# Kernel tuning notes

Measured on AMD Instinct MI355X. Metric: run time of the kernel, lower is better.

## Reference

```python
import jax, jax.numpy as jnp
import numpy as np

B = 32768
INPUT_DIM = 2048
D = 2
HIDDEN = 128
V = 20          # output_dim (number of heads)
P = 6           # n_corr_params
R = 10          # r_lora = min(V // 2, 10)


def setup_inputs() -> dict:
    key = jax.random.key(0)
    ks = jax.random.split(key, 12)

    def lin(k, fan_in, shape):
        bound = 1.0 / np.sqrt(fan_in)
        return jax.random.uniform(k, shape, jnp.float32, -bound, bound)

    x = jax.random.normal(ks[0], (B, INPUT_DIM), jnp.float32)
    # encoder: Linear(input_dim, hidden) -> ReLU -> (Dropout=id) -> Linear(hidden, d)
    We1 = lin(ks[1], INPUT_DIM, (INPUT_DIM, HIDDEN))
    be1 = lin(ks[2], INPUT_DIM, (HIDDEN,))
    We2 = lin(ks[3], HIDDEN, (HIDDEN, D))
    be2 = lin(ks[4], HIDDEN, (D,))
    # 20 heads, each Linear(d, hidden) -> ReLU -> Linear(hidden, 6) -> Tanh,
    # stacked into batched weight tensors.
    W1 = lin(ks[5], D, (V, D, HIDDEN))
    b1 = lin(ks[6], D, (V, HIDDEN))
    W2 = lin(ks[7], HIDDEN, (V, HIDDEN, P))
    b2 = lin(ks[8], HIDDEN, (V, P))
    # LoRA params
    lora_A = jax.random.normal(ks[9], (D, R), jnp.float32) * 0.01
    lora_B = jax.random.normal(ks[10], (R, V * P), jnp.float32) * 0.01
    return {"x": x, "We1": We1, "be1": be1, "We2": We2, "be2": be2,
            "W1": W1, "b1": b1, "W2": W2, "b2": b2,
            "lora_A": lora_A, "lora_B": lora_B}


def reference(x, We1, be1, We2, be2, W1, b1, W2, b2, lora_A, lora_B):
    # encoder (nonlinear reduction; dropout is identity in eval)
    z = jax.nn.relu(x @ We1 + be1) @ We2 + be2            # [B, D]
    # all 20 heads as batched GEMMs
    h = jax.nn.relu(jnp.einsum('bd,vdh->bvh', z, W1) + b1)  # [B, V, HIDDEN]
    heads = jnp.tanh(jnp.einsum('bvh,vhp->bvp', h, W2) + b2)  # [B, V, P]
    # LoRA contribution, then outer tanh (note: double tanh, faithful to source)
    lora = (z @ lora_A @ lora_B).reshape(-1, V, P)         # [B, V, P]
    out = jnp.tanh(heads + 0.15 * lora)
    return (out, z)
```

## Files before the change

### kernel.cpp

```cpp
#include <hip/hip_runtime.h>
#include <hip/hip_bf16.h>
#include <cstdint>
#include <cstddef>

#define BDIM   32768
#define KDIM   2048
#define NDIM   128
#define VHEADS 20
#define PDIM   6
#define RLORA  10

#define BK      64
#define NCHUNK  (KDIM / BK)
#define OUT_ELEMS   (BDIM * VHEADS * PDIM)
#define WS_W_BYTES  (KDIM * NDIM * 2)

typedef __attribute__((ext_vector_type(8))) __bf16 bf16x8;
typedef __attribute__((ext_vector_type(4))) float f32x4;
typedef __attribute__((ext_vector_type(2))) float f32x2;
typedef __attribute__((ext_vector_type(4))) unsigned int u32x4;

union FragU { bf16x8 b; u32x4 u; };

__device__ __forceinline__ unsigned int cvt_pk_bf16(float lo, float hi) {
  unsigned int r;
  asm("v_cvt_pk_bf16_f32 %0, %1, %2" : "=v"(r) : "v"(lo), "v"(hi));
  return r;
}

__device__ __forceinline__ void gload_lds16(const void* g, void* l) {
  __builtin_amdgcn_global_load_lds(
      (const __attribute__((address_space(1))) void*)(g),
      (__attribute__((address_space(3))) void*)(l), 16, 0, 0);
}

__device__ __forceinline__ float fast_tanh(float x) {
  float ax = fabsf(x);
  float e  = __expf(-2.0f * ax);
  float t  = __fdividef(1.0f - e, 1.0f + e);
  return copysignf(t, x);
}

__global__ __launch_bounds__(256)
void k0_pack(const float* __restrict__ We1,
             const float* __restrict__ lA,
             const float* __restrict__ lB,
             unsigned short* __restrict__ wsw,
             float* __restrict__ wsM) {
  if (blockIdx.x == 128) {
    int t = threadIdx.x;
    if (t < 2 * VHEADS * PDIM) {
      int d  = t / (VHEADS * PDIM);
      int vp = t - d * (VHEADS * PDIM);
      float s = 0.f;
#pragma unroll
      for (int r = 0; r < RLORA; ++r)
        s = fmaf(lA[d * RLORA + r], lB[r * (VHEADS * PDIM) + vp], s);
      wsM[t] = s;
    }
    return;
  }
  int t    = blockIdx.x * 256 + threadIdx.x;
  int lane = t & 63;
  int blk  = t >> 6;
  int ks   = blk & 1;
  int nt   = (blk >> 1) & 7;
  int c    = blk >> 4;
  int n    = nt * 16 + (lane & 15);
  int kb   = c * BK + ks * 32 + (lane >> 4) * 8;

  unsigned int u[4];
#pragma unroll
  for (int q = 0; q < 4; ++q) {
    float f0 = We1[(size_t)(kb + 2 * q + 0) * NDIM + n];
    float f1 = We1[(size_t)(kb + 2 * q + 1) * NDIM + n];
    __hip_bfloat16 h0 = __float2bfloat16(f0);
    __hip_bfloat16 h1 = __float2bfloat16(f1);
    u[q] = (unsigned int)*reinterpret_cast<unsigned short*>(&h0) |
           ((unsigned int)*reinterpret_cast<unsigned short*>(&h1) << 16);
  }
  *reinterpret_cast<u32x4*>(wsw + (size_t)t * 8) = u32x4{u[0], u[1], u[2], u[3]};
}

__global__ __launch_bounds__(256, 2)
void k1_fused(const float* __restrict__ x,
              const unsigned short* __restrict__ wp,
              const float* __restrict__ be1,
              const float* __restrict__ We2,
              const float* __restrict__ be2,
              const float* __restrict__ W1,
              const float* __restrict__ b1,
              const float* __restrict__ W2,
              const float* __restrict__ b2,
              const float* __restrict__ M,
              float* __restrict__ out,
              float* __restrict__ zout) {
  __shared__ char ldsA[2][16384] __attribute__((aligned(16)));
  __shared__ char ldsB[2][16384] __attribute__((aligned(16)));
  __shared__ float zsh[64][2];

  const int tid  = threadIdx.x;
  const int lane = tid & 63;
  const int wv   = tid >> 6;
  const int l15  = lane & 15;
  const int kgrp = lane >> 4;
  const int blk  = blockIdx.x;

  const int arow_off = wv * 16 + (lane >> 4);
  const char* bsrc = (const char*)wp + lane * 16;

  f32x4 acc[8];
#pragma unroll
  for (int i = 0; i < 8; ++i) acc[i] = f32x4{0.f, 0.f, 0.f, 0.f};

  auto STAGE = [&](int b, int c) {
#pragma unroll
    for (int q = 0; q < 4; ++q) {
      int row = arow_off + q * 4;
      const float* asrc = x + ((size_t)(blk * 64 + row) * KDIM + c * BK
                               + (((l15 ^ (row & 7)) << 2)));
      gload_lds16(asrc, &ldsA[b][(wv * 4 + q) * 1024]);
    }
#pragma unroll
    for (int q = 0; q < 4; ++q) {
      gload_lds16(bsrc + (size_t)c * 16384 + (wv * 4 + q) * 1024,
                  &ldsB[b][(wv * 4 + q) * 1024]);
    }
  };

  auto COMPUTE = [&](int b) {
    const int row = wv * 16 + l15;
    const char* abase = &ldsA[b][row * 256];
    const int rx = (row & 7) << 4;
    f32x4 A0 = *(const f32x4*)(abase + (((kgrp * 2 + 0) << 4) ^ rx));
    f32x4 A1 = *(const f32x4*)(abase + (((kgrp * 2 + 1) << 4) ^ rx));
    f32x4 A2 = *(const f32x4*)(abase + 128 + (((kgrp * 2 + 0) << 4) ^ rx));
    f32x4 A3 = *(const f32x4*)(abase + 128 + (((kgrp * 2 + 1) << 4) ^ rx));
    FragU a0, a1;
    a0.u = u32x4{cvt_pk_bf16(A0.x, A0.y), cvt_pk_bf16(A0.z, A0.w),
                 cvt_pk_bf16(A1.x, A1.y), cvt_pk_bf16(A1.z, A1.w)};
    a1.u = u32x4{cvt_pk_bf16(A2.x, A2.y), cvt_pk_bf16(A2.z, A2.w),
                 cvt_pk_bf16(A3.x, A3.y), cvt_pk_bf16(A3.z, A3.w)};
    const char* bbase = &ldsB[b][lane * 16];
#pragma unroll
    for (int nt = 0; nt < 8; ++nt) {
      FragU b0, b1;
      b0.u = *(const u32x4*)(bbase + (nt * 2 + 0) * 1024);
      b1.u = *(const u32x4*)(bbase + (nt * 2 + 1) * 1024);
      acc[nt] = __builtin_amdgcn_mfma_f32_16x16x32_bf16(a0.b, b0.b, acc[nt], 0, 0, 0);
      acc[nt] = __builtin_amdgcn_mfma_f32_16x16x32_bf16(a1.b, b1.b, acc[nt], 0, 0, 0);
    }
  };

  STAGE(0, 0);
  __syncthreads();

#pragma unroll 2
  for (int c = 0; c < NCHUNK; ++c) {
    int b = c & 1;
    if (c + 1 < NCHUNK) STAGE(b ^ 1, c + 1);
    COMPUTE(b);
    __syncthreads();
  }

  float part[4][2];
#pragma unroll
  for (int j = 0; j < 4; ++j) { part[j][0] = 0.f; part[j][1] = 0.f; }
#pragma unroll
  for (int nt = 0; nt < 8; ++nt) {
    int col = nt * 16 + l15;
    float bb = be1[col];
    float w0 = We2[col * 2 + 0];
    float w1 = We2[col * 2 + 1];
#pragma unroll
    for (int j = 0; j < 4; ++j) {
      float h = acc[nt][j] + bb;
      h = h > 0.f ? h : 0.f;
      part[j][0] = fmaf(h, w0, part[j][0]);
      part[j][1] = fmaf(h, w1, part[j][1]);
    }
  }
#pragma unroll
  for (int m = 1; m < 16; m <<= 1) {
#pragma unroll
    for (int j = 0; j < 4; ++j) {
      part[j][0] += __shfl_xor(part[j][0], m, 64);
      part[j][1] += __shfl_xor(part[j][1], m, 64);
    }
  }
  if (l15 == 0) {
    float bz0 = be2[0], bz1 = be2[1];
#pragma unroll
    for (int j = 0; j < 4; ++j) {
      int rl = wv * 16 + kgrp * 4 + j;
      float zz0 = part[j][0] + bz0;
      float zz1 = part[j][1] + bz1;
      zsh[rl][0] = zz0;
      zsh[rl][1] = zz1;
      f32x2 zz = {zz0, zz1};
      *(f32x2*)(zout + (size_t)(blk * 64 + rl) * 2) = zz;
    }
  }
  __syncthreads();

  const int wvu = __builtin_amdgcn_readfirstlane(wv);
  float z0 = zsh[lane][0];
  float z1 = zsh[lane][1];
  float* orow = out + (size_t)(blk * 64 + lane) * (VHEADS * PDIM);

#pragma unroll 1
  for (int i = 0; i < 5; ++i) {
    int v = i * 4 + wvu;
    const float* w1a = W1 + (size_t)(v * 2 + 0) * NDIM;
    const float* w1b = W1 + (size_t)(v * 2 + 1) * NDIM;
    const float* bb1 = b1 + (size_t)v * NDIM;
    const float* w2  = W2 + (size_t)v * NDIM * PDIM;

    float p[6] = {0.f, 0.f, 0.f, 0.f, 0.f, 0.f};
#pragma unroll 4
    for (int h = 0; h < NDIM; ++h) {
      float hv = fmaf(z0, w1a[h], fmaf(z1, w1b[h], bb1[h]));
      hv = hv > 0.f ? hv : 0.f;
#pragma unroll
      for (int j = 0; j < 6; ++j) p[j] = fmaf(hv, w2[h * 6 + j], p[j]);
    }
    float o[6];
#pragma unroll
    for (int j = 0; j < 6; ++j) {
      float t1 = fast_tanh(p[j] + b2[v * PDIM + j]);
      float lo = fmaf(z0, M[v * PDIM + j], z1 * M[VHEADS * PDIM + v * PDIM + j]);
      o[j] = fast_tanh(fmaf(0.15f, lo, t1));
    }
    float* op = orow + v * PDIM;
    f32x2 o01 = {o[0], o[1]};
    f32x2 o23 = {o[2], o[3]};
    f32x2 o45 = {o[4], o[5]};
    __builtin_nontemporal_store(o01, (f32x2*)(op + 0));
    __builtin_nontemporal_store(o23, (f32x2*)(op + 2));
    __builtin_nontemporal_store(o45, (f32x2*)(op + 4));
  }
}

extern "C" void kernel_launch(void* const* d_in, const int* in_sizes, int n_in,
                              void* d_out, int out_size, void* d_ws, size_t ws_size,
                              hipStream_t stream) {
  const float* x   = (const float*)d_in[0];
  const float* We1 = (const float*)d_in[1];
  const float* be1 = (const float*)d_in[2];
  const float* We2 = (const float*)d_in[3];
  const float* be2 = (const float*)d_in[4];
  const float* W1  = (const float*)d_in[5];
  const float* b1  = (const float*)d_in[6];
  const float* W2  = (const float*)d_in[7];
  const float* b2  = (const float*)d_in[8];
  const float* lA  = (const float*)d_in[9];
  const float* lB  = (const float*)d_in[10];

  float* out  = (float*)d_out;
  float* zout = out + OUT_ELEMS;
  unsigned short* wsw = (unsigned short*)d_ws;
  float* wsM = (float*)((char*)d_ws + WS_W_BYTES);

  hipLaunchKernelGGL(k0_pack, dim3(129), dim3(256), 0, stream,
                     We1, lA, lB, wsw, wsM);
  hipLaunchKernelGGL(k1_fused, dim3(BDIM / 64), dim3(256), 0, stream,
                     x, wsw, be1, We2, be2, W1, b1, W2, b2, wsM, out, zout);
}
```

Measured before the change: 116.9 us.

## Shrink row tile to 16 and split hidden columns across waves with direct B loads

Reduces the per-block row tile from 64 to 16 rows, giving 2048 blocks, and splits the 128 hidden columns across the four waves, each wave holding two 16-column accumulators. The packed bf16 weights are now read straight from global memory into registers instead of being staged through LDS. The K chunk grows to 128. Per-wave partial z values are reduced through shared memory, and the head stage spreads the 20 heads over 16 slots of 16 rows. The aim is more occupancy and parallelism with less LDS traffic, at the cost of re-reading the weight matrix from L2 four times as often and adding an extra cross-wave reduction barrier.

```diff
diff --git a/kernel.cpp b/kernel.cpp
--- a/kernel.cpp
+++ b/kernel.cpp
@@ -10,8 +10,9 @@
 #define PDIM   6
 #define RLORA  10
 
-#define BK      64
-#define NCHUNK  (KDIM / BK)
+#define BM     16
+#define BK2    128
+#define NCH    (KDIM / BK2)
 #define OUT_ELEMS   (BDIM * VHEADS * PDIM)
 #define WS_W_BYTES  (KDIM * NDIM * 2)
 
@@ -67,7 +68,7 @@
   int nt   = (blk >> 1) & 7;
   int c    = blk >> 4;
   int n    = nt * 16 + (lane & 15);
-  int kb   = c * BK + ks * 32 + (lane >> 4) * 8;
+  int kb   = c * 64 + ks * 32 + (lane >> 4) * 8;
 
   unsigned int u[4];
 #pragma unroll
@@ -82,7 +83,7 @@
   *reinterpret_cast<u32x4*>(wsw + (size_t)t * 8) = u32x4{u[0], u[1], u[2], u[3]};
 }
 
-__global__ __launch_bounds__(256, 2)
+__global__ __launch_bounds__(256, 4)
 void k1_fused(const float* __restrict__ x,
               const unsigned short* __restrict__ wp,
               const float* __restrict__ be1,
@@ -95,9 +96,9 @@
               const float* __restrict__ M,
               float* __restrict__ out,
               float* __restrict__ zout) {
-  __shared__ char ldsA[2][16384] __attribute__((aligned(16)));
-  __shared__ char ldsB[2][16384] __attribute__((aligned(16)));
-  __shared__ float zsh[64][2];
+  __shared__ float ldsA[2][2048] __attribute__((aligned(16)));
+  __shared__ float zpart[4][16][2];
+  __shared__ float zsh[16][2];
 
   const int tid  = threadIdx.x;
   const int lane = tid & 63;
@@ -106,60 +107,56 @@
   const int kgrp = lane >> 4;
   const int blk  = blockIdx.x;
 
-  const int arow_off = wv * 16 + (lane >> 4);
-  const char* bsrc = (const char*)wp + lane * 16;
-
-  f32x4 acc[8];
-#pragma unroll
-  for (int i = 0; i < 8; ++i) acc[i] = f32x4{0.f, 0.f, 0.f, 0.f};
+  const float* arow = x + (size_t)(blk * BM + wv * 4 + (lane >> 4)) * KDIM
+                        + (lane & 15) * 4;
+
+  f32x4 acc[2];
+  acc[0] = f32x4{0.f, 0.f, 0.f, 0.f};
+  acc[1] = f32x4{0.f, 0.f, 0.f, 0.f};
 
   auto STAGE = [&](int b, int c) {
-#pragma unroll
-    for (int q = 0; q < 4; ++q) {
-      int row = arow_off + q * 4;
-      const float* asrc = x + ((size_t)(blk * 64 + row) * KDIM + c * BK
-                               + (((l15 ^ (row & 7)) << 2)));
-      gload_lds16(asrc, &ldsA[b][(wv * 4 + q) * 1024]);
-    }
-#pragma unroll
-    for (int q = 0; q < 4; ++q) {
-      gload_lds16(bsrc + (size_t)c * 16384 + (wv * 4 + q) * 1024,
-                  &ldsB[b][(wv * 4 + q) * 1024]);
-    }
+    const float* s0 = arow + c * BK2;
+    gload_lds16(s0,      &ldsA[b][wv * 256]);
+    gload_lds16(s0 + 64, &ldsA[b][1024 + wv * 256]);
   };
 
-  auto COMPUTE = [&](int b) {
-    const int row = wv * 16 + l15;
-    const char* abase = &ldsA[b][row * 256];
-    const int rx = (row & 7) << 4;
-    f32x4 A0 = *(const f32x4*)(abase + (((kgrp * 2 + 0) << 4) ^ rx));
-    f32x4 A1 = *(const f32x4*)(abase + (((kgrp * 2 + 1) << 4) ^ rx));
-    f32x4 A2 = *(const f32x4*)(abase + 128 + (((kgrp * 2 + 0) << 4) ^ rx));
-    f32x4 A3 = *(const f32x4*)(abase + 128 + (((kgrp * 2 + 1) << 4) ^ rx));
-    FragU a0, a1;
-    a0.u = u32x4{cvt_pk_bf16(A0.x, A0.y), cvt_pk_bf16(A0.z, A0.w),
-                 cvt_pk_bf16(A1.x, A1.y), cvt_pk_bf16(A1.z, A1.w)};
-    a1.u = u32x4{cvt_pk_bf16(A2.x, A2.y), cvt_pk_bf16(A2.z, A2.w),
-                 cvt_pk_bf16(A3.x, A3.y), cvt_pk_bf16(A3.z, A3.w)};
-    const char* bbase = &ldsB[b][lane * 16];
-#pragma unroll
-    for (int nt = 0; nt < 8; ++nt) {
-      FragU b0, b1;
-      b0.u = *(const u32x4*)(bbase + (nt * 2 + 0) * 1024);
-      b1.u = *(const u32x4*)(bbase + (nt * 2 + 1) * 1024);
-      acc[nt] = __builtin_amdgcn_mfma_f32_16x16x32_bf16(a0.b, b0.b, acc[nt], 0, 0, 0);
-      acc[nt] = __builtin_amdgcn_mfma_f32_16x16x32_bf16(a1.b, b1.b, acc[nt], 0, 0, 0);
+  auto COMPUTE = [&](int b, int c) {
+    const char* bb = (const char*)wp + (size_t)c * 32768 + lane * 16;
+    FragU bf[2][4];
+#pragma unroll
+    for (int ntl = 0; ntl < 2; ++ntl) {
+      int nt = wv * 2 + ntl;
+#pragma unroll
+      for (int ks = 0; ks < 4; ++ks) {
+        int off = (((ks >> 1) * 16) + nt * 2 + (ks & 1)) * 1024;
+        bf[ntl][ks].u = *(const u32x4*)(bb + off);
+      }
+    }
+    const char* ab = (const char*)&ldsA[b][0] + l15 * 256 + kgrp * 32;
+    FragU af[4];
+#pragma unroll
+    for (int ks = 0; ks < 4; ++ks) {
+      const char* p = ab + (ks & 1) * 128 + (ks >> 1) * 4096;
+      f32x4 lo = *(const f32x4*)(p);
+      f32x4 hi = *(const f32x4*)(p + 16);
+      af[ks].u = u32x4{cvt_pk_bf16(lo.x, lo.y), cvt_pk_bf16(lo.z, lo.w),
+                       cvt_pk_bf16(hi.x, hi.y), cvt_pk_bf16(hi.z, hi.w)};
+    }
+#pragma unroll
+    for (int ks = 0; ks < 4; ++ks) {
+      acc[0] = __builtin_amdgcn_mfma_f32_16x16x32_bf16(af[ks].b, bf[0][ks].b, acc[0], 0, 0, 0);
+      acc[1] = __builtin_amdgcn_mfma_f32_16x16x32_bf16(af[ks].b, bf[1][ks].b, acc[1], 0, 0, 0);
     }
   };
 
   STAGE(0, 0);
   __syncthreads();
 
-#pragma unroll 2
-  for (int c = 0; c < NCHUNK; ++c) {
+#pragma unroll 1
+  for (int c = 0; c < NCH; ++c) {
     int b = c & 1;
-    if (c + 1 < NCHUNK) STAGE(b ^ 1, c + 1);
-    COMPUTE(b);
+    if (c + 1 < NCH) STAGE(b ^ 1, c + 1);
+    COMPUTE(b, c);
     __syncthreads();
   }
 
@@ -167,14 +164,14 @@
 #pragma unroll
   for (int j = 0; j < 4; ++j) { part[j][0] = 0.f; part[j][1] = 0.f; }
 #pragma unroll
-  for (int nt = 0; nt < 8; ++nt) {
-    int col = nt * 16 + l15;
+  for (int ntl = 0; ntl < 2; ++ntl) {
+    int col = (wv * 2 + ntl) * 16 + l15;
     float bb = be1[col];
     float w0 = We2[col * 2 + 0];
     float w1 = We2[col * 2 + 1];
 #pragma unroll
     for (int j = 0; j < 4; ++j) {
-      float h = acc[nt][j] + bb;
+      float h = acc[ntl][j] + bb;
       h = h > 0.f ? h : 0.f;
       part[j][0] = fmaf(h, w0, part[j][0]);
       part[j][1] = fmaf(h, w1, part[j][1]);
@@ -189,28 +186,32 @@
     }
   }
   if (l15 == 0) {
-    float bz0 = be2[0], bz1 = be2[1];
 #pragma unroll
     for (int j = 0; j < 4; ++j) {
-      int rl = wv * 16 + kgrp * 4 + j;
-      float zz0 = part[j][0] + bz0;
-      float zz1 = part[j][1] + bz1;
-      zsh[rl][0] = zz0;
-      zsh[rl][1] = zz1;
-      f32x2 zz = {zz0, zz1};
-      *(f32x2*)(zout + (size_t)(blk * 64 + rl) * 2) = zz;
+      zpart[wv][kgrp * 4 + j][0] = part[j][0];
+      zpart[wv][kgrp * 4 + j][1] = part[j][1];
     }
   }
   __syncthreads();
-
-  const int wvu = __builtin_amdgcn_readfirstlane(wv);
-  float z0 = zsh[lane][0];
-  float z1 = zsh[lane][1];
-  float* orow = out + (size_t)(blk * 64 + lane) * (VHEADS * PDIM);
-
-#pragma unroll 1
-  for (int i = 0; i < 5; ++i) {
-    int v = i * 4 + wvu;
+  if (tid < BM) {
+    float s0 = zpart[0][tid][0] + zpart[1][tid][0] + zpart[2][tid][0] +
+               zpart[3][tid][0] + be2[0];
+    float s1 = zpart[0][tid][1] + zpart[1][tid][1] + zpart[2][tid][1] +
+               zpart[3][tid][1] + be2[1];
+    zsh[tid][0] = s0;
+    zsh[tid][1] = s1;
+    f32x2 zz = {s0, s1};
+    *(f32x2*)(zout + (size_t)(blk * BM + tid) * 2) = zz;
+  }
+  __syncthreads();
+
+  const int srow = tid & 15;
+  const int slot = tid >> 4;
+  float z0 = zsh[srow][0];
+  float z1 = zsh[srow][1];
+  float* orow = out + (size_t)(blk * BM + srow) * (VHEADS * PDIM);
+
+  auto head = [&](int v) {
     const float* w1a = W1 + (size_t)(v * 2 + 0) * NDIM;
     const float* w1b = W1 + (size_t)(v * 2 + 1) * NDIM;
     const float* bb1 = b1 + (size_t)v * NDIM;
@@ -238,7 +239,10 @@
     __builtin_nontemporal_store(o01, (f32x2*)(op + 0));
     __builtin_nontemporal_store(o23, (f32x2*)(op + 2));
     __builtin_nontemporal_store(o45, (f32x2*)(op + 4));
-  }
+  };
+
+  head(slot);
+  if (slot < 4) head(16 + slot);
 }
 
 extern "C" void kernel_launch(void* const* d_in, const int* in_sizes, int n_in,
@@ -263,6 +267,6 @@
 
   hipLaunchKernelGGL(k0_pack, dim3(129), dim3(256), 0, stream,
                      We1, lA, lB, wsw, wsM);
-  hipLaunchKernelGGL(k1_fused, dim3(BDIM / 64), dim3(256), 0, stream,
+  hipLaunchKernelGGL(k1_fused, dim3(BDIM / BM), dim3(256), 0, stream,
                      x, wsw, be1, We2, be2, W1, b1, W2, b2, wsM, out, zout);
 }
```

New measurement: 152.8 us. +30.7%, slower.

## Split GEMM tile across 8 waves with column halves and rebalance head loop

Applied to the files above, without the earlier changes.

Doubles the block size to 512 threads, arranging waves as 4 row groups by 2 column halves so each wave accumulates 16x64 instead of 16x128, with a shared-memory reduction to combine z partials. Staging loads are redistributed over all threads and the per-head epilogue is spread across 8 waves. The intent is more waves in flight to hide global-to-LDS latency and to cut register pressure, at the cost of an extra barrier and a cross-wave reduction.

```diff
diff --git a/kernel.cpp b/kernel.cpp
--- a/kernel.cpp
+++ b/kernel.cpp
@@ -67,7 +67,7 @@
   int nt   = (blk >> 1) & 7;
   int c    = blk >> 4;
   int n    = nt * 16 + (lane & 15);
-  int kb   = c * BK + ks * 32 + (lane >> 4) * 8;
+  int kb   = c * 64 + ks * 32 + (lane >> 4) * 8;
 
   unsigned int u[4];
 #pragma unroll
@@ -82,7 +82,7 @@
   *reinterpret_cast<u32x4*>(wsw + (size_t)t * 8) = u32x4{u[0], u[1], u[2], u[3]};
 }
 
-__global__ __launch_bounds__(256, 2)
+__global__ __launch_bounds__(512, 4)
 void k1_fused(const float* __restrict__ x,
               const unsigned short* __restrict__ wp,
               const float* __restrict__ be1,
@@ -97,39 +97,40 @@
               float* __restrict__ zout) {
   __shared__ char ldsA[2][16384] __attribute__((aligned(16)));
   __shared__ char ldsB[2][16384] __attribute__((aligned(16)));
+  __shared__ float zpart2[64][2][2];
   __shared__ float zsh[64][2];
 
   const int tid  = threadIdx.x;
   const int lane = tid & 63;
   const int wv   = tid >> 6;
+  const int wr   = wv & 3;
+  const int wc   = wv >> 2;
   const int l15  = lane & 15;
   const int kgrp = lane >> 4;
   const int blk  = blockIdx.x;
 
-  const int arow_off = wv * 16 + (lane >> 4);
-  const char* bsrc = (const char*)wp + lane * 16;
-
-  f32x4 acc[8];
-#pragma unroll
-  for (int i = 0; i < 8; ++i) acc[i] = f32x4{0.f, 0.f, 0.f, 0.f};
+  f32x4 acc[4];
+#pragma unroll
+  for (int i = 0; i < 4; ++i) acc[i] = f32x4{0.f, 0.f, 0.f, 0.f};
 
   auto STAGE = [&](int b, int c) {
 #pragma unroll
-    for (int q = 0; q < 4; ++q) {
-      int row = arow_off + q * 4;
-      const float* asrc = x + ((size_t)(blk * 64 + row) * KDIM + c * BK
-                               + (((l15 ^ (row & 7)) << 2)));
-      gload_lds16(asrc, &ldsA[b][(wv * 4 + q) * 1024]);
-    }
-#pragma unroll
-    for (int q = 0; q < 4; ++q) {
-      gload_lds16(bsrc + (size_t)c * 16384 + (wv * 4 + q) * 1024,
-                  &ldsB[b][(wv * 4 + q) * 1024]);
+    for (int q = 0; q < 2; ++q) {
+      int s = tid + q * 512;
+      int row = s >> 4;
+      int g = (s & 15) ^ (row & 7);
+      const float* asrc = x + (size_t)(blk * 64 + row) * KDIM + c * BK + g * 4;
+      gload_lds16(asrc, &ldsA[b][s * 16]);
+    }
+#pragma unroll
+    for (int q = 0; q < 2; ++q) {
+      gload_lds16((const char*)wp + (size_t)c * 16384 + q * 8192 + tid * 16,
+                  &ldsB[b][q * 8192 + tid * 16]);
     }
   };
 
   auto COMPUTE = [&](int b) {
-    const int row = wv * 16 + l15;
+    const int row = wr * 16 + l15;
     const char* abase = &ldsA[b][row * 256];
     const int rx = (row & 7) << 4;
     f32x4 A0 = *(const f32x4*)(abase + (((kgrp * 2 + 0) << 4) ^ rx));
@@ -143,10 +144,10 @@
                  cvt_pk_bf16(A3.x, A3.y), cvt_pk_bf16(A3.z, A3.w)};
     const char* bbase = &ldsB[b][lane * 16];
 #pragma unroll
-    for (int nt = 0; nt < 8; ++nt) {
+    for (int nt = 0; nt < 4; ++nt) {
       FragU b0, b1;
-      b0.u = *(const u32x4*)(bbase + (nt * 2 + 0) * 1024);
-      b1.u = *(const u32x4*)(bbase + (nt * 2 + 1) * 1024);
+      b0.u = *(const u32x4*)(bbase + ((wc * 4 + nt) * 2 + 0) * 1024);
+      b1.u = *(const u32x4*)(bbase + ((wc * 4 + nt) * 2 + 1) * 1024);
       acc[nt] = __builtin_amdgcn_mfma_f32_16x16x32_bf16(a0.b, b0.b, acc[nt], 0, 0, 0);
       acc[nt] = __builtin_amdgcn_mfma_f32_16x16x32_bf16(a1.b, b1.b, acc[nt], 0, 0, 0);
     }
@@ -155,7 +156,7 @@
   STAGE(0, 0);
   __syncthreads();
 
-#pragma unroll 2
+#pragma unroll 1
   for (int c = 0; c < NCHUNK; ++c) {
     int b = c & 1;
     if (c + 1 < NCHUNK) STAGE(b ^ 1, c + 1);
@@ -167,8 +168,8 @@
 #pragma unroll
   for (int j = 0; j < 4; ++j) { part[j][0] = 0.f; part[j][1] = 0.f; }
 #pragma unroll
-  for (int nt = 0; nt < 8; ++nt) {
-    int col = nt * 16 + l15;
+  for (int nt = 0; nt < 4; ++nt) {
+    int col = (wc * 4 + nt) * 16 + l15;
     float bb = be1[col];
     float w0 = We2[col * 2 + 0];
     float w1 = We2[col * 2 + 1];
@@ -189,17 +190,21 @@
     }
   }
   if (l15 == 0) {
-    float bz0 = be2[0], bz1 = be2[1];
 #pragma unroll
     for (int j = 0; j < 4; ++j) {
-      int rl = wv * 16 + kgrp * 4 + j;
-      float zz0 = part[j][0] + bz0;
-      float zz1 = part[j][1] + bz1;
-      zsh[rl][0] = zz0;
-      zsh[rl][1] = zz1;
-      f32x2 zz = {zz0, zz1};
-      *(f32x2*)(zout + (size_t)(blk * 64 + rl) * 2) = zz;
-    }
+      int rl = wr * 16 + kgrp * 4 + j;
+      zpart2[rl][wc][0] = part[j][0];
+      zpart2[rl][wc][1] = part[j][1];
+    }
+  }
+  __syncthreads();
+  if (tid < 64) {
+    float s0 = zpart2[tid][0][0] + zpart2[tid][1][0] + be2[0];
+    float s1 = zpart2[tid][0][1] + zpart2[tid][1][1] + be2[1];
+    zsh[tid][0] = s0;
+    zsh[tid][1] = s1;
+    f32x2 zz = {s0, s1};
+    *(f32x2*)(zout + (size_t)(blk * 64 + tid) * 2) = zz;
   }
   __syncthreads();
 
@@ -208,9 +213,7 @@
   float z1 = zsh[lane][1];
   float* orow = out + (size_t)(blk * 64 + lane) * (VHEADS * PDIM);
 
-#pragma unroll 1
-  for (int i = 0; i < 5; ++i) {
-    int v = i * 4 + wvu;
+  auto head = [&](int v) {
     const float* w1a = W1 + (size_t)(v * 2 + 0) * NDIM;
     const float* w1b = W1 + (size_t)(v * 2 + 1) * NDIM;
     const float* bb1 = b1 + (size_t)v * NDIM;
@@ -238,7 +241,11 @@
     __builtin_nontemporal_store(o01, (f32x2*)(op + 0));
     __builtin_nontemporal_store(o23, (f32x2*)(op + 2));
     __builtin_nontemporal_store(o45, (f32x2*)(op + 4));
-  }
+  };
+
+  head(wvu);
+  head(wvu + 8);
+  if (wvu < 4) head(wvu + 16);
 }
 
 extern "C" void kernel_launch(void* const* d_in, const int* in_sizes, int n_in,
@@ -263,6 +270,6 @@
 
   hipLaunchKernelGGL(k0_pack, dim3(129), dim3(256), 0, stream,
                      We1, lA, lB, wsw, wsM);
-  hipLaunchKernelGGL(k1_fused, dim3(BDIM / 64), dim3(256), 0, stream,
+  hipLaunchKernelGGL(k1_fused, dim3(BDIM / 64), dim3(512), 0, stream,
                      x, wsw, be1, We2, be2, W1, b1, W2, b2, wsM, out, zout);
 }
```

Result: faster. 102.7 us (-12.2%).
